# Optimization experiments

Measured on AMD Instinct MI355X. Metric: run time of the kernel, lower is better.

The kernel has to match this reference:

```python
import jax, jax.numpy as jnp
import numpy as np

B, HW, ENC, DEC, ATTN = 512, 196, 2048, 512, 512

def setup_inputs() -> dict:
    key = jax.random.key(0)
    ks = jax.random.split(key, 8)
    s_enc = 1.0 / np.sqrt(ENC)
    s_dec = 1.0 / np.sqrt(DEC)
    s_v = 1.0 / np.sqrt(ATTN)
    return {
        "enc_out": jax.random.normal(ks[0], (B, HW, ENC), dtype=jnp.float32),
        "dec_h": jax.random.normal(ks[1], (B, DEC), dtype=jnp.float32),
        "W_enc": jax.random.uniform(ks[2], (ENC, ATTN), jnp.float32, -s_enc, s_enc),
        "b_enc": jax.random.uniform(ks[3], (ATTN,), jnp.float32, -s_enc, s_enc),
        "W_dec": jax.random.uniform(ks[4], (DEC, ATTN), jnp.float32, -s_dec, s_dec),
        "b_dec": jax.random.uniform(ks[5], (ATTN,), jnp.float32, -s_dec, s_dec),
        "W_v": jax.random.uniform(ks[6], (ATTN,), jnp.float32, -s_v, s_v),
        "b_v": jax.random.uniform(ks[7], (), jnp.float32, -s_v, s_v),
    }

def reference(enc_out, dec_h, W_enc, b_enc, W_dec, b_dec, W_v, b_v):
    # attn1: [B, HW, ATTN]; attn2: [B, 1, ATTN]
    attn1 = jnp.einsum('bse,ea->bsa', enc_out, W_enc) + b_enc
    attn2 = (dec_h @ W_dec + b_dec)[:, None, :]
    score = jax.nn.relu(attn1 + attn2)
    logits = jnp.einsum('bsa,a->bs', score, W_v) + b_v  # [B, HW]
    alpha = jax.nn.softmax(logits, axis=1)
    context_vec = jnp.einsum('bs,bse->be', alpha, enc_out)
    return (context_vec, alpha)
```

## Files before the change

### kernel.cpp

```cpp
#include <hip/hip_runtime.h>
#include <hip/hip_bf16.h>
#include <cstdint>
#include <cstddef>

#define B_    512
#define HW_   196
#define ENC_  2048
#define DEC_  512
#define ATTN_ 512
#define M_    (B_*HW_)

typedef __attribute__((ext_vector_type(8))) short short8;
typedef __attribute__((ext_vector_type(4))) float f32x4;

__device__ __forceinline__ unsigned short f2bf(float x) {
  __bf16 b = (__bf16)x;
  return __builtin_bit_cast(unsigned short, b);
}
__device__ __forceinline__ unsigned int cvt2(float x, float y) {
  return (unsigned)f2bf(x) | ((unsigned)f2bf(y) << 16);
}

__device__ __forceinline__ void gload_lds16(const void* g, void* l) {
  __builtin_amdgcn_global_load_lds(
      (const __attribute__((address_space(1))) void*)g,
      (__attribute__((address_space(3))) void*)l, 16, 0, 0);
}

__global__ __launch_bounds__(256)
void k_convert(const float* __restrict__ in, unsigned short* __restrict__ out) {
  const size_t total  = (size_t)M_ * ENC_;
  const size_t stride = (size_t)gridDim.x * 256 * 8;
  for (size_t i = ((size_t)blockIdx.x * 256 + threadIdx.x) * 8; i < total; i += stride) {
    const float4 a = *reinterpret_cast<const float4*>(in + i);
    const float4 b = *reinterpret_cast<const float4*>(in + i + 4);
    uint4 o;
    o.x = cvt2(a.x, a.y);  o.y = cvt2(a.z, a.w);
    o.z = cvt2(b.x, b.y);  o.w = cvt2(b.z, b.w);
    *reinterpret_cast<uint4*>(out + i) = o;
  }
}

__global__ __launch_bounds__(256)
void k_attn2(const float* __restrict__ dec_h, const float* __restrict__ Wdec,
             const float* __restrict__ bdec, const float* __restrict__ benc,
             float* __restrict__ attn2p) {
  __shared__ float dh[DEC_];
  const int b = blockIdx.x;
  const int t = threadIdx.x;
  dh[t]       = dec_h[b*DEC_ + t];
  dh[t + 256] = dec_h[b*DEC_ + t + 256];
  __syncthreads();
  #pragma unroll
  for (int rep = 0; rep < 2; ++rep) {
    const int a = t + rep*256;
    float acc = bdec[a] + benc[a];
    #pragma unroll 8
    for (int k = 0; k < DEC_; ++k)
      acc = fmaf(dh[k], Wdec[(size_t)k*ATTN_ + a], acc);
    attn2p[(size_t)b*ATTN_ + a] = acc;
  }
}

__global__ __launch_bounds__(256)
void k_transpose(const float* __restrict__ Wenc, unsigned short* __restrict__ WencT) {
  __shared__ float tile[32][33];
  const int e0 = blockIdx.x * 32;
  const int a0 = blockIdx.y * 32;
  const int t  = threadIdx.x;
  const int li = t >> 5;
  const int lj = t & 31;
  #pragma unroll
  for (int rep = 0; rep < 4; ++rep) {
    const int i = li + rep*8;
    tile[i][lj] = Wenc[(size_t)(e0 + i)*ATTN_ + a0 + lj];
  }
  __syncthreads();
  #pragma unroll
  for (int rep = 0; rep < 4; ++rep) {
    const int ar = li + rep*8;
    WencT[(size_t)(a0 + ar)*ENC_ + e0 + lj] = f2bf(tile[lj][ar]);
  }
}

#define NKS 64

__global__ __launch_bounds__(512, 1)
void k_gemm8(const unsigned short* __restrict__ ench,
             const unsigned short* __restrict__ WencT,
             const float* __restrict__ attn2p,
             const float* __restrict__ Wv,
             float* __restrict__ partials) {
  __shared__ unsigned short A3[3][256*32];
  __shared__ unsigned short B3[3][256*32];

  const int tid = threadIdx.x;
  const int id  = blockIdx.x;
  const int xcd  = id & 7;
  const int rest = id >> 3;
  const int nb   = rest & 1;
  const int mblk = (rest >> 1)*8 + xcd;
  const int r0 = mblk * 256;
  const int n0 = nb * 256;

  const int w  = tid >> 6;
  const int l  = tid & 63;
  const int wm = w >> 2, wn = w & 3;
  const int lrow = l & 15;
  const int kg   = l >> 4;

  const unsigned short* aSrc[2];
  const unsigned short* bSrc[2];
  #pragma unroll
  for (int i = 0; i < 2; ++i) {
    const int j  = tid + i*512;
    const int rr = j >> 2;
    const int kc = (j & 3) ^ ((rr >> 1) & 3);
    aSrc[i] = ench  + (size_t)(r0 + rr)*ENC_ + kc*8;
    bSrc[i] = WencT + (size_t)(n0 + rr)*ENC_ + kc*8;
  }

  int aOff[8], bOff[4];
  #pragma unroll
  for (int mi = 0; mi < 8; ++mi) {
    const int R = wm*128 + mi*16 + lrow;
    aOff[mi] = (R*4 + (kg ^ ((R >> 1) & 3))) * 8;
  }
  #pragma unroll
  for (int ni = 0; ni < 4; ++ni) {
    const int C = wn*64 + ni*16 + lrow;
    bOff[ni] = (C*4 + (kg ^ ((C >> 1) & 3))) * 8;
  }

  f32x4 acc[8][4];
  #pragma unroll
  for (int mi = 0; mi < 8; ++mi)
    #pragma unroll
    for (int ni = 0; ni < 4; ++ni)
      acc[mi][ni] = (f32x4){0.f, 0.f, 0.f, 0.f};

#define STAGE(KT) do {                                                         \
    const size_t _ko = (size_t)(KT)*32;                                        \
    const int _bw = (KT) % 3;                                                  \
    gload_lds16(aSrc[0] + _ko, &A3[_bw][tid*8]);                               \
    gload_lds16(aSrc[1] + _ko, &A3[_bw][4096 + tid*8]);                        \
    gload_lds16(bSrc[0] + _ko, &B3[_bw][tid*8]);                               \
    gload_lds16(bSrc[1] + _ko, &B3[_bw][4096 + tid*8]);                        \
  } while (0)

  STAGE(0); STAGE(1);
  asm volatile("s_waitcnt vmcnt(4)" ::: "memory");
  __builtin_amdgcn_s_barrier();

  for (int kt = 0; kt < NKS; ++kt) {
    const unsigned short* aB = &A3[kt % 3][0];
    const unsigned short* bB = &B3[kt % 3][0];

    __builtin_amdgcn_s_setprio(1);
    short8 aF[4], bF[4], aG[4];
    #pragma unroll
    for (int mi = 0; mi < 4; ++mi)
      aF[mi] = *reinterpret_cast<const short8*>(&aB[aOff[mi]]);
    #pragma unroll
    for (int ni = 0; ni < 4; ++ni)
      bF[ni] = *reinterpret_cast<const short8*>(&bB[bOff[ni]]);
    #pragma unroll
    for (int mi = 0; mi < 4; ++mi)
      aG[mi] = *reinterpret_cast<const short8*>(&aB[aOff[4 + mi]]);
    #pragma unroll
    for (int mi = 0; mi < 4; ++mi)
      #pragma unroll
      for (int ni = 0; ni < 4; ++ni)
        acc[mi][ni] = __builtin_amdgcn_mfma_f32_16x16x32_bf16(
            aF[mi], bF[ni], acc[mi][ni], 0, 0, 0);
    #pragma unroll
    for (int mi = 0; mi < 4; ++mi)
      #pragma unroll
      for (int ni = 0; ni < 4; ++ni)
        acc[4 + mi][ni] = __builtin_amdgcn_mfma_f32_16x16x32_bf16(
            aG[mi], bF[ni], acc[4 + mi][ni], 0, 0, 0);
    __builtin_amdgcn_s_setprio(0);

    if (kt + 2 < NKS) STAGE(kt + 2);

    asm volatile("s_waitcnt lgkmcnt(0)" ::: "memory");
    if (kt < NKS - 3)       { asm volatile("s_waitcnt vmcnt(4)" ::: "memory"); }
    else if (kt == NKS - 2) { asm volatile("s_waitcnt vmcnt(0)" ::: "memory"); }
    __builtin_amdgcn_s_barrier();
  }
#undef STAGE

  __syncthreads();
  float* plog = reinterpret_cast<float*>(&A3[0][0]);
  float wvv[4];
  #pragma unroll
  for (int ni = 0; ni < 4; ++ni) wvv[ni] = Wv[n0 + wn*64 + ni*16 + lrow];
  #pragma unroll
  for (int mi = 0; mi < 8; ++mi) {
    #pragma unroll
    for (int j = 0; j < 4; ++j) {
      const int row_local = wm*128 + mi*16 + kg*4 + j;
      const int r  = r0 + row_local;
      const int bb = r / HW_;
      const float* a2 = attn2p + (size_t)bb*ATTN_ + n0 + wn*64;
      float s = 0.f;
      #pragma unroll
      for (int ni = 0; ni < 4; ++ni) {
        float v = acc[mi][ni][j] + a2[ni*16 + lrow];
        v = fmaxf(v, 0.f);
        s = fmaf(v, wvv[ni], s);
      }
      s += __shfl_xor(s, 1);
      s += __shfl_xor(s, 2);
      s += __shfl_xor(s, 4);
      s += __shfl_xor(s, 8);
      if (lrow == 0) plog[row_local*4 + wn] = s;
    }
  }
  __syncthreads();
  if (tid < 256) {
    const float4 p = *reinterpret_cast<const float4*>(&plog[tid*4]);
    partials[(size_t)(r0 + tid)*2 + nb] = p.x + p.y + p.z + p.w;
  }
}

#define BM 128
#define BN 128
#define BK 32
#define LDA 40
#define NT (ENC_/BK)
__device__ __forceinline__ int invswz8(int p) {
  const int b2 = ((p >> 2) ^ (p >> 4)) & 1;
  const int b1 = ((p >> 1) ^ (p >> 3)) & 1;
  const int b0 = (p ^ (p >> 2) ^ (p >> 4)) & 1;
  return (p & ~7) | (b2 << 2) | (b1 << 1) | b0;
}
__global__ __launch_bounds__(256)
void k_gemm_logits_f32(const float* __restrict__ enc,
                       const unsigned short* __restrict__ WencT,
                       const float* __restrict__ attn2p,
                       const float* __restrict__ Wv,
                       float* __restrict__ partials) {
  __shared__ unsigned short As[BM*LDA];
  __shared__ unsigned short Bs[2][BN*BK];
  __shared__ float plog[BM][2];
  const int tid  = threadIdx.x;
  const int id   = blockIdx.x;
  const int xcd  = id & 7;
  const int rest = id >> 3;
  const int nb   = rest & 3;
  const int mblk = (rest >> 2) * 8 + xcd;
  const int r0 = mblk * BM;
  const int n0 = nb * BN;
  const int arow  = tid >> 1;
  const int ahalf = (tid & 1) << 4;
  const float* aptr = enc + (size_t)(r0 + arow)*ENC_ + ahalf;
  const unsigned short* bbase = WencT + (size_t)n0*ENC_;
  const int w  = tid >> 6;
  const int l  = tid & 63;
  const int wm = w >> 1, wn = w & 1;
  const int lrow = l & 15;
  const int kg   = l >> 4;
  const int lk8  = kg << 3;
  const int g4   = kg << 2;
  f32x4 acc[4][4];
  #pragma unroll
  for (int mi = 0; mi < 4; ++mi)
    #pragma unroll
    for (int ni = 0; ni < 4; ++ni)
      acc[mi][ni] = (f32x4){0.f, 0.f, 0.f, 0.f};
  float4 ar[4];
  #pragma unroll
  for (int i = 0; i < 4; ++i) ar[i] = *reinterpret_cast<const float4*>(aptr + i*4);
  #pragma unroll
  for (int r = 0; r < 2; ++r) {
    const int p = r*256 + tid;
    const int c = invswz8(p);
    gload_lds16(bbase + (size_t)(c >> 2)*ENC_ + (c & 3)*8, &Bs[0][p*8]);
  }
  for (int kt = 0; kt < NT; ++kt) {
    {
      unsigned int pk[8];
      #pragma unroll
      for (int i = 0; i < 4; ++i) {
        pk[2*i]   = cvt2(ar[i].x, ar[i].y);
        pk[2*i+1] = cvt2(ar[i].z, ar[i].w);
      }
      uint4* da = reinterpret_cast<uint4*>(&As[arow*LDA + ahalf]);
      da[0] = make_uint4(pk[0], pk[1], pk[2], pk[3]);
      da[1] = make_uint4(pk[4], pk[5], pk[6], pk[7]);
    }
    __syncthreads();
    if (kt + 1 < NT) {
      const float* ap = aptr + (kt + 1)*BK;
      #pragma unroll
      for (int i = 0; i < 4; ++i) ar[i] = *reinterpret_cast<const float4*>(ap + i*4);
      const int k0n = (kt + 1)*BK;
      unsigned short* bdst = Bs[(kt + 1) & 1];
      #pragma unroll
      for (int r = 0; r < 2; ++r) {
        const int p = r*256 + tid;
        const int c = invswz8(p);
        gload_lds16(bbase + (size_t)(c >> 2)*ENC_ + k0n + (c & 3)*8, &bdst[p*8]);
      }
    }
    const unsigned short* bsc = Bs[kt & 1];
    short8 aF[4], bF[4];
    #pragma unroll
    for (int mi = 0; mi < 4; ++mi)
      aF[mi] = *reinterpret_cast<const short8*>(&As[(wm*64 + mi*16 + lrow)*LDA + lk8]);
    #pragma unroll
    for (int ni = 0; ni < 4; ++ni) {
      const int cr = ((wn*64 + ni*16 + lrow) << 2) + kg;
      const int pr = cr ^ ((cr >> 2) & 7);
      bF[ni] = *reinterpret_cast<const short8*>(&bsc[pr << 3]);
    }
    #pragma unroll
    for (int mi = 0; mi < 4; ++mi)
      #pragma unroll
      for (int ni = 0; ni < 4; ++ni)
        acc[mi][ni] = __builtin_amdgcn_mfma_f32_16x16x32_bf16(aF[mi], bF[ni], acc[mi][ni], 0, 0, 0);
    __syncthreads();
  }
  float wvv[4];
  #pragma unroll
  for (int ni = 0; ni < 4; ++ni) wvv[ni] = Wv[n0 + wn*64 + ni*16 + lrow];
  #pragma unroll
  for (int mi = 0; mi < 4; ++mi) {
    #pragma unroll
    for (int j = 0; j < 4; ++j) {
      const int row_local = wm*64 + mi*16 + g4 + j;
      const int r  = r0 + row_local;
      const int bb = r / HW_;
      const float* a2 = attn2p + (size_t)bb*ATTN_ + n0 + wn*64;
      float s = 0.f;
      #pragma unroll
      for (int ni = 0; ni < 4; ++ni) {
        float v = acc[mi][ni][j] + a2[ni*16 + lrow];
        v = fmaxf(v, 0.f);
        s = fmaf(v, wvv[ni], s);
      }
      s += __shfl_xor(s, 1);
      s += __shfl_xor(s, 2);
      s += __shfl_xor(s, 4);
      s += __shfl_xor(s, 8);
      if (lrow == 0) plog[row_local][wn] = s;
    }
  }
  __syncthreads();
  if (tid < BM)
    partials[(size_t)(r0 + tid)*4 + nb] = plog[tid][0] + plog[tid][1];
}

__global__ __launch_bounds__(64)
void k_softmax2(const float* __restrict__ partials, const float* __restrict__ bvp,
                float* __restrict__ alpha) {
  const int b = blockIdx.x;
  const int t = threadIdx.x;
  const float bv = bvp[0];
  float lg[4];
  #pragma unroll
  for (int i = 0; i < 4; ++i) {
    const int s = t + i*64;
    if (s < HW_) {
      const float2 p = *reinterpret_cast<const float2*>(&partials[(size_t)(b*HW_ + s)*2]);
      lg[i] = p.x + p.y + bv;
    } else lg[i] = -INFINITY;
  }
  float mx = fmaxf(fmaxf(lg[0], lg[1]), fmaxf(lg[2], lg[3]));
  #pragma unroll
  for (int off = 32; off; off >>= 1) mx = fmaxf(mx, __shfl_xor(mx, off));
  float sum = 0.f;
  #pragma unroll
  for (int i = 0; i < 4; ++i) { lg[i] = expf(lg[i] - mx); sum += lg[i]; }
  #pragma unroll
  for (int off = 32; off; off >>= 1) sum += __shfl_xor(sum, off);
  const float inv = 1.0f / sum;
  #pragma unroll
  for (int i = 0; i < 4; ++i) {
    const int s = t + i*64;
    if (s < HW_) alpha[b*HW_ + s] = lg[i] * inv;
  }
}

__global__ __launch_bounds__(64)
void k_softmax4(const float* __restrict__ partials, const float* __restrict__ bvp,
                float* __restrict__ alpha) {
  const int b = blockIdx.x;
  const int t = threadIdx.x;
  const float bv = bvp[0];
  float lg[4];
  #pragma unroll
  for (int i = 0; i < 4; ++i) {
    const int s = t + i*64;
    if (s < HW_) {
      const float4 p = *reinterpret_cast<const float4*>(&partials[(size_t)(b*HW_ + s)*4]);
      lg[i] = p.x + p.y + p.z + p.w + bv;
    } else lg[i] = -INFINITY;
  }
  float mx = fmaxf(fmaxf(lg[0], lg[1]), fmaxf(lg[2], lg[3]));
  #pragma unroll
  for (int off = 32; off; off >>= 1) mx = fmaxf(mx, __shfl_xor(mx, off));
  float sum = 0.f;
  #pragma unroll
  for (int i = 0; i < 4; ++i) { lg[i] = expf(lg[i] - mx); sum += lg[i]; }
  #pragma unroll
  for (int off = 32; off; off >>= 1) sum += __shfl_xor(sum, off);
  const float inv = 1.0f / sum;
  #pragma unroll
  for (int i = 0; i < 4; ++i) {
    const int s = t + i*64;
    if (s < HW_) alpha[b*HW_ + s] = lg[i] * inv;
  }
}

__global__ __launch_bounds__(256)
void k_context_bf16(const unsigned short* __restrict__ ench,
                    const float* __restrict__ alpha, float* __restrict__ ctx) {
  __shared__ float al[HW_];
  const int b = blockIdx.x;
  const int t = threadIdx.x;
  if (t < HW_) al[t] = alpha[b*HW_ + t];
  __syncthreads();
  const unsigned short* base = ench + (size_t)b*HW_*ENC_ + t*8;
  float acc[8] = {0.f,0.f,0.f,0.f,0.f,0.f,0.f,0.f};
  #pragma unroll 2
  for (int s = 0; s < HW_; ++s) {
    const uint4 v = *reinterpret_cast<const uint4*>(base + (size_t)s*ENC_);
    const float a = al[s];
    const unsigned u[4] = {v.x, v.y, v.z, v.w};
    #pragma unroll
    for (int q = 0; q < 4; ++q) {
      const float lo = __builtin_bit_cast(float, u[q] << 16);
      const float hi = __builtin_bit_cast(float, u[q] & 0xffff0000u);
      acc[2*q]   = fmaf(a, lo, acc[2*q]);
      acc[2*q+1] = fmaf(a, hi, acc[2*q+1]);
    }
  }
  float4* o = reinterpret_cast<float4*>(&ctx[(size_t)b*ENC_ + t*8]);
  o[0] = make_float4(acc[0], acc[1], acc[2], acc[3]);
  o[1] = make_float4(acc[4], acc[5], acc[6], acc[7]);
}

__global__ __launch_bounds__(256)
void k_context_f32(const float* __restrict__ enc, const float* __restrict__ alpha,
                   float* __restrict__ ctx) {
  __shared__ float al[HW_];
  const int bi = blockIdx.x;
  const int b  = bi >> 1;
  const int e0 = (bi & 1) << 10;
  const int t  = threadIdx.x;
  if (t < HW_) al[t] = alpha[b*HW_ + t];
  __syncthreads();
  const float* base = enc + (size_t)b*HW_*ENC_ + e0 + t*4;
  float4 acc = {0.f, 0.f, 0.f, 0.f};
  #pragma unroll 4
  for (int s = 0; s < HW_; ++s) {
    const float a = al[s];
    const float4 v = *reinterpret_cast<const float4*>(base + (size_t)s*ENC_);
    acc.x = fmaf(a, v.x, acc.x);
    acc.y = fmaf(a, v.y, acc.y);
    acc.z = fmaf(a, v.z, acc.z);
    acc.w = fmaf(a, v.w, acc.w);
  }
  *reinterpret_cast<float4*>(&ctx[(size_t)b*ENC_ + e0 + t*4]) = acc;
}

extern "C" void kernel_launch(void* const* d_in, const int* in_sizes, int n_in,
                              void* d_out, int out_size, void* d_ws, size_t ws_size,
                              hipStream_t stream) {
  const float* enc   = (const float*)d_in[0];
  const float* dec_h = (const float*)d_in[1];
  const float* Wenc  = (const float*)d_in[2];
  const float* benc  = (const float*)d_in[3];
  const float* Wdec  = (const float*)d_in[4];
  const float* bdec  = (const float*)d_in[5];
  const float* Wv    = (const float*)d_in[6];
  const float* bv    = (const float*)d_in[7];

  float* ctx   = (float*)d_out;
  float* alpha = (float*)d_out + (size_t)B_*ENC_;

  char* ws = (char*)d_ws;
  float*          attn2p   = (float*)ws;
  unsigned short* WencT    = (unsigned short*)(ws + (1u << 20));
  float*          partials = (float*)(ws + 3u*(1u << 20));
  unsigned short* ench     = (unsigned short*)(ws + 5u*(1u << 20));
  const size_t needed = 5u*(1u << 20) + (size_t)M_*ENC_*sizeof(unsigned short);
  const bool big = (ws_size >= needed);

  hipLaunchKernelGGL(k_attn2,     dim3(B_),                dim3(256), 0, stream,
                     dec_h, Wdec, bdec, benc, attn2p);
  hipLaunchKernelGGL(k_transpose, dim3(ENC_/32, ATTN_/32), dim3(256), 0, stream,
                     Wenc, WencT);
  if (big) {
    hipLaunchKernelGGL(k_convert,   dim3(2048),            dim3(256), 0, stream,
                       enc, ench);
    hipLaunchKernelGGL(k_gemm8,     dim3(784),             dim3(512), 0, stream,
                       ench, WencT, attn2p, Wv, partials);
    hipLaunchKernelGGL(k_softmax2,  dim3(B_),              dim3(64),  0, stream,
                       partials, bv, alpha);
    hipLaunchKernelGGL(k_context_bf16, dim3(B_),           dim3(256), 0, stream,
                       ench, alpha, ctx);
  } else {
    hipLaunchKernelGGL(k_gemm_logits_f32, dim3(3136),      dim3(256), 0, stream,
                       enc, WencT, attn2p, Wv, partials);
    hipLaunchKernelGGL(k_softmax4,  dim3(B_),              dim3(64),  0, stream,
                       partials, bv, alpha);
    hipLaunchKernelGGL(k_context_f32, dim3(1024),          dim3(256), 0, stream,
                       enc, alpha, ctx);
  }
}
```

Baseline: 689.9 us.

## Shrink bf16 GEMM tile to 256x128 with 256 threads and two blocks per CU

Reshapes the fused logits GEMM from a 256x256 tile run by 512 threads at one block per CU into a 256x128 tile run by 256 threads. The goal is two resident blocks per CU, twice as many blocks in the grid, and less LDS per block, so one block's barriers and loads can overlap with the other's work. Each wave keeps the same 128x64 sub-tile, so register use per wave is unchanged. The cost is that every A tile is now loaded twice, raising global and L2 traffic. Partials now come in four column slices, so the four-way softmax kernel replaces the two-way one.

```diff
diff --git a/kernel.cpp b/kernel.cpp
--- a/kernel.cpp
+++ b/kernel.cpp
@@ -85,38 +85,44 @@
 
 #define NKS 64
 
-__global__ __launch_bounds__(512, 1)
+__global__ __launch_bounds__(256, 2)
 void k_gemm8(const unsigned short* __restrict__ ench,
              const unsigned short* __restrict__ WencT,
              const float* __restrict__ attn2p,
              const float* __restrict__ Wv,
              float* __restrict__ partials) {
   __shared__ unsigned short A3[3][256*32];
-  __shared__ unsigned short B3[3][256*32];
+  __shared__ unsigned short B3[3][128*32];
 
   const int tid = threadIdx.x;
   const int id  = blockIdx.x;
   const int xcd  = id & 7;
   const int rest = id >> 3;
-  const int nb   = rest & 1;
-  const int mblk = (rest >> 1)*8 + xcd;
+  const int nb   = rest & 3;
+  const int mblk = (rest >> 2)*8 + xcd;
   const int r0 = mblk * 256;
-  const int n0 = nb * 256;
+  const int n0 = nb * 128;
 
   const int w  = tid >> 6;
   const int l  = tid & 63;
-  const int wm = w >> 2, wn = w & 3;
+  const int wm = w >> 1, wn = w & 1;
   const int lrow = l & 15;
   const int kg   = l >> 4;
 
-  const unsigned short* aSrc[2];
-  const unsigned short* bSrc[2];
-  #pragma unroll
-  for (int i = 0; i < 2; ++i) {
-    const int j  = tid + i*512;
+  const unsigned short* aSrc[4];
+  #pragma unroll
+  for (int i = 0; i < 4; ++i) {
+    const int j  = tid + i*256;
     const int rr = j >> 2;
     const int kc = (j & 3) ^ ((rr >> 1) & 3);
-    aSrc[i] = ench  + (size_t)(r0 + rr)*ENC_ + kc*8;
+    aSrc[i] = ench + (size_t)(r0 + rr)*ENC_ + kc*8;
+  }
+  const unsigned short* bSrc[2];
+  #pragma unroll
+  for (int i = 0; i < 2; ++i) {
+    const int j  = tid + i*256;
+    const int rr = j >> 2;
+    const int kc = (j & 3) ^ ((rr >> 1) & 3);
     bSrc[i] = WencT + (size_t)(n0 + rr)*ENC_ + kc*8;
   }
 
@@ -143,13 +149,15 @@
     const size_t _ko = (size_t)(KT)*32;                                        \
     const int _bw = (KT) % 3;                                                  \
     gload_lds16(aSrc[0] + _ko, &A3[_bw][tid*8]);                               \
-    gload_lds16(aSrc[1] + _ko, &A3[_bw][4096 + tid*8]);                        \
+    gload_lds16(aSrc[1] + _ko, &A3[_bw][2048 + tid*8]);                        \
+    gload_lds16(aSrc[2] + _ko, &A3[_bw][4096 + tid*8]);                        \
+    gload_lds16(aSrc[3] + _ko, &A3[_bw][6144 + tid*8]);                        \
     gload_lds16(bSrc[0] + _ko, &B3[_bw][tid*8]);                               \
-    gload_lds16(bSrc[1] + _ko, &B3[_bw][4096 + tid*8]);                        \
+    gload_lds16(bSrc[1] + _ko, &B3[_bw][2048 + tid*8]);                        \
   } while (0)
 
   STAGE(0); STAGE(1);
-  asm volatile("s_waitcnt vmcnt(4)" ::: "memory");
+  asm volatile("s_waitcnt vmcnt(6)" ::: "memory");
   __builtin_amdgcn_s_barrier();
 
   for (int kt = 0; kt < NKS; ++kt) {
@@ -184,7 +192,7 @@
     if (kt + 2 < NKS) STAGE(kt + 2);
 
     asm volatile("s_waitcnt lgkmcnt(0)" ::: "memory");
-    if (kt < NKS - 3)       { asm volatile("s_waitcnt vmcnt(4)" ::: "memory"); }
+    if (kt <= NKS - 3)      { asm volatile("s_waitcnt vmcnt(6)" ::: "memory"); }
     else if (kt == NKS - 2) { asm volatile("s_waitcnt vmcnt(0)" ::: "memory"); }
     __builtin_amdgcn_s_barrier();
   }
@@ -214,14 +222,12 @@
       s += __shfl_xor(s, 2);
       s += __shfl_xor(s, 4);
       s += __shfl_xor(s, 8);
-      if (lrow == 0) plog[row_local*4 + wn] = s;
-    }
-  }
-  __syncthreads();
-  if (tid < 256) {
-    const float4 p = *reinterpret_cast<const float4*>(&plog[tid*4]);
-    partials[(size_t)(r0 + tid)*2 + nb] = p.x + p.y + p.z + p.w;
-  }
+      if (lrow == 0) plog[row_local*2 + wn] = s;
+    }
+  }
+  __syncthreads();
+  if (tid < 256)
+    partials[(size_t)(r0 + tid)*4 + nb] = plog[tid*2] + plog[tid*2 + 1];
 }
 
 #define BM 128
@@ -353,37 +359,6 @@
 }
 
 __global__ __launch_bounds__(64)
-void k_softmax2(const float* __restrict__ partials, const float* __restrict__ bvp,
-                float* __restrict__ alpha) {
-  const int b = blockIdx.x;
-  const int t = threadIdx.x;
-  const float bv = bvp[0];
-  float lg[4];
-  #pragma unroll
-  for (int i = 0; i < 4; ++i) {
-    const int s = t + i*64;
-    if (s < HW_) {
-      const float2 p = *reinterpret_cast<const float2*>(&partials[(size_t)(b*HW_ + s)*2]);
-      lg[i] = p.x + p.y + bv;
-    } else lg[i] = -INFINITY;
-  }
-  float mx = fmaxf(fmaxf(lg[0], lg[1]), fmaxf(lg[2], lg[3]));
-  #pragma unroll
-  for (int off = 32; off; off >>= 1) mx = fmaxf(mx, __shfl_xor(mx, off));
-  float sum = 0.f;
-  #pragma unroll
-  for (int i = 0; i < 4; ++i) { lg[i] = expf(lg[i] - mx); sum += lg[i]; }
-  #pragma unroll
-  for (int off = 32; off; off >>= 1) sum += __shfl_xor(sum, off);
-  const float inv = 1.0f / sum;
-  #pragma unroll
-  for (int i = 0; i < 4; ++i) {
-    const int s = t + i*64;
-    if (s < HW_) alpha[b*HW_ + s] = lg[i] * inv;
-  }
-}
-
-__global__ __launch_bounds__(64)
 void k_softmax4(const float* __restrict__ partials, const float* __restrict__ bvp,
                 float* __restrict__ alpha) {
   const int b = blockIdx.x;
@@ -496,9 +471,9 @@
   if (big) {
     hipLaunchKernelGGL(k_convert,   dim3(2048),            dim3(256), 0, stream,
                        enc, ench);
-    hipLaunchKernelGGL(k_gemm8,     dim3(784),             dim3(512), 0, stream,
+    hipLaunchKernelGGL(k_gemm8,     dim3(1568),            dim3(256), 0, stream,
                        ench, WencT, attn2p, Wv, partials);
-    hipLaunchKernelGGL(k_softmax2,  dim3(B_),              dim3(64),  0, stream,
+    hipLaunchKernelGGL(k_softmax4,  dim3(B_),              dim3(64),  0, stream,
                        partials, bv, alpha);
     hipLaunchKernelGGL(k_context_bf16, dim3(B_),           dim3(256), 0, stream,
                        ench, alpha, ctx);
```

New measurement: 672.0 us. 2.6% less time.
